# Kernel tuning notes

Measured on AMD Instinct MI355X. Metric: run time of the kernel, lower is better.

Reference implementation:

```python
import jax, jax.numpy as jnp
import numpy as np

B, T, C, H = 8, 2048, 1024, 128

def setup_inputs() -> dict:
    key = jax.random.key(0)
    kx, kq, kk, kv = jax.random.split(key, 4)
    x = jax.random.normal(kx, (B, T, C), dtype=jnp.float32)
    # torch nn.Linear(C, H, bias=False) computes x @ W.T with W of shape [H, C];
    # we store the transposed [C, H] matrices directly.
    Wq = jax.random.normal(kq, (C, H), dtype=jnp.float32) * (C ** -0.5)
    Wk = jax.random.normal(kk, (C, H), dtype=jnp.float32) * (C ** -0.5)
    Wv = jax.random.normal(kv, (C, H), dtype=jnp.float32) * (C ** -0.5)
    return {"x": x, "Wq": Wq, "Wk": Wk, "Wv": Wv}

def reference(x, Wq, Wk, Wv):
    # x: [B,T,C]; projections: [B,T,H]
    q = jnp.einsum('btc,ch->bth', x, Wq)
    k = jnp.einsum('btc,ch->bth', x, Wk)
    v = jnp.einsum('btc,ch->bth', x, Wv)
    scale = k.shape[-1] ** -0.5
    wei = jnp.einsum('bth,bsh->bts', q, k) * scale          # [B,T,T]
    # causal mask: position t attends to s <= t
    causal = jnp.tril(jnp.ones((x.shape[1], x.shape[1]), dtype=bool))
    wei = jnp.where(causal, wei, -jnp.inf)
    wei = jax.nn.softmax(wei, axis=-1)
    # dropout p=0.0 -> identity
    out = jnp.einsum('bts,bsh->bth', wei, v)                # [B,T,H]
    return out
```

## Files before the change

### kernel.cpp

```cpp
#include <hip/hip_runtime.h>
#include <hip/hip_bf16.h>

#define DB 8
#define DT 2048
#define DC 1024
#define DH 128

typedef __attribute__((ext_vector_type(8))) short short8;
typedef __attribute__((ext_vector_type(4))) float f32x4;
typedef __attribute__((ext_vector_type(4))) int i32x4;
typedef __attribute__((ext_vector_type(4))) unsigned short u16x4;

static __device__ __forceinline__ unsigned short bfbits(float x){
    union { float f; unsigned u; } a; a.f = x;
    unsigned u = a.u;
    unsigned r = u + 0x7fffu + ((u >> 16) & 1u);
    return (unsigned short)(r >> 16);
}
static __device__ __forceinline__ unsigned pbf2(float lo, float hi){
    return (unsigned)bfbits(lo) | ((unsigned)bfbits(hi) << 16);
}
static __device__ __forceinline__ float bf2f(unsigned short u){
    union { unsigned u; float f; } t; t.u = ((unsigned)u) << 16; return t.f;
}

static __device__ __forceinline__ short8 redist(unsigned pk0, unsigned pk1,
                                                unsigned pk2, unsigned pk3,
                                                int g, int c){
    const int src0 = c + (((2*g    ) & 3) << 4);
    const int src1 = c + (((2*g + 1) & 3) << 4);
    const int sel  = g >> 1;
    unsigned a0 = __shfl(pk0, src0), a2 = __shfl(pk2, src0);
    unsigned b0 = __shfl(pk1, src0), b2 = __shfl(pk3, src0);
    unsigned c0 = __shfl(pk0, src1), c2 = __shfl(pk2, src1);
    unsigned d0 = __shfl(pk1, src1), d2 = __shfl(pk3, src1);
    i32x4 pw = { (int)(sel ? a2 : a0), (int)(sel ? b2 : b0),
                 (int)(sel ? c2 : c0), (int)(sel ? d2 : d0) };
    return __builtin_bit_cast(short8, pw);
}

__global__ __launch_bounds__(256) void prep_wt_kernel(const float* __restrict__ Wq,
                                                      const float* __restrict__ Wk,
                                                      const float* __restrict__ Wv,
                                                      unsigned short* __restrict__ WTc){
    int gid = blockIdx.x * 256 + threadIdx.x;
    int e  = gid & 7;
    int F3 = gid >> 3;
    int n  = F3 % 384;
    int ct = F3 / 384;
    int k  = (ct >> 2) * 32 + (ct & 3) * 8 + e;
    int p  = n >> 7, h = n & 127;
    const float* W = (p == 0) ? Wq : (p == 1 ? Wk : Wv);
    float v = W[(size_t)k * DH + h];
    if (p == 0) v *= 0.08838834764831845f * 1.4426950408889634f;
    WTc[gid] = bfbits(v);
}

__global__ __launch_bounds__(512, 4) void qkv_kernel(const float* __restrict__ x,
                                                     const unsigned short* __restrict__ WTc,
                                                     unsigned short* __restrict__ Qb,
                                                     unsigned short* __restrict__ Kb,
                                                     unsigned short* __restrict__ VT){
    __shared__ unsigned short Bs[2][12288];
    __shared__ unsigned short As[2][2560];

    const int tid  = threadIdx.x;
    const int lane = tid & 63;
    const int w    = tid >> 6;
    const int g = lane >> 4, c = lane & 15;
    const int m0 = blockIdx.x * 64;
    const int n0 = w * 48;

    const unsigned short* bsrc = WTc + (size_t)tid * 8;
    const bool doA = tid < 256;
    const int arow = tid >> 2, ac8 = tid & 3;
    const float* asrc = x + (size_t)(m0 + arow) * DC + ac8 * 8;

    f32x4 acc[4][3] = {};
    i32x4 breg[3];
    float4 av0, av1;

#pragma unroll
    for (int j = 0; j < 3; ++j)
        breg[j] = *(const i32x4*)(bsrc + j * 4096);
    if (doA){ av0 = *(const float4*)asrc; av1 = *(const float4*)(asrc + 4); }
#pragma unroll
    for (int j = 0; j < 3; ++j)
        *(i32x4*)(&Bs[0][j * 4096 + tid * 8]) = breg[j];
    if (doA){
        i32x4 h8 = { (int)pbf2(av0.x, av0.y), (int)pbf2(av0.z, av0.w),
                     (int)pbf2(av1.x, av1.y), (int)pbf2(av1.z, av1.w) };
        *(i32x4*)(&As[0][arow * 40 + ac8 * 8]) = h8;
    }

    for (int t = 0; t < DC / 32; ++t){
        const int cur = t & 1;
        __syncthreads();
        if (t < DC / 32 - 1){
#pragma unroll
            for (int j = 0; j < 3; ++j)
                breg[j] = *(const i32x4*)(bsrc + (t + 1) * 12288 + j * 4096);
            if (doA){
                av0 = *(const float4*)(asrc + (t + 1) * 32);
                av1 = *(const float4*)(asrc + (t + 1) * 32 + 4);
            }
        }
        short8 af[4], bfr[3];
#pragma unroll
        for (int mf = 0; mf < 4; ++mf)
            af[mf] = *(const short8*)(&As[cur][(mf*16 + c) * 40 + g * 8]);
#pragma unroll
        for (int nf = 0; nf < 3; ++nf)
            bfr[nf] = *(const short8*)(&Bs[cur][g * 3072 + (n0 + nf*16 + c) * 8]);
#pragma unroll
        for (int mf = 0; mf < 4; ++mf)
#pragma unroll
            for (int nf = 0; nf < 3; ++nf)
                acc[mf][nf] = __builtin_amdgcn_mfma_f32_16x16x32_bf16(af[mf], bfr[nf], acc[mf][nf], 0, 0, 0);
        if (t < DC / 32 - 1){
#pragma unroll
            for (int j = 0; j < 3; ++j)
                *(i32x4*)(&Bs[cur ^ 1][j * 4096 + tid * 8]) = breg[j];
            if (doA){
                i32x4 h8 = { (int)pbf2(av0.x, av0.y), (int)pbf2(av0.z, av0.w),
                             (int)pbf2(av1.x, av1.y), (int)pbf2(av1.z, av1.w) };
                *(i32x4*)(&As[cur ^ 1][arow * 40 + ac8 * 8]) = h8;
            }
        }
    }

    const int bb = m0 >> 11;
    const int tb = m0 & 2047;
#pragma unroll
    for (int mf = 0; mf < 4; ++mf)
#pragma unroll
        for (int nf = 0; nf < 3; ++nf){
            const int n  = n0 + nf*16;
            const int p  = n >> 7;
            const int np = (n & 127) + c;
            const int row = m0 + mf*16 + 4*g;
            if (p < 2){
                unsigned short* O = (p == 0) ? Qb : Kb;
#pragma unroll
                for (int r = 0; r < 4; ++r)
                    O[(size_t)(row + r) * DH + np] = bfbits(acc[mf][nf][r]);
            } else {
                const int t0 = tb + mf*16 + 4*g;
                u16x4 v = { bfbits(acc[mf][nf][0]), bfbits(acc[mf][nf][1]),
                            bfbits(acc[mf][nf][2]), bfbits(acc[mf][nf][3]) };
                *(u16x4*)(VT + ((size_t)bb * DH + np) * DT + t0) = v;
            }
        }
}

__global__ __launch_bounds__(256, 2) void attn_kernel(const unsigned short* __restrict__ Qb,
                                                      const unsigned short* __restrict__ Kb,
                                                      const unsigned short* __restrict__ VT,
                                                      unsigned short* __restrict__ OP,
                                                      float* __restrict__ ML){
    __shared__ unsigned char lds[32768];

    const int tid  = threadIdx.x;
    const int lane = tid & 63;
    const int w    = tid >> 6;
    const int g = lane >> 4, c = lane & 15;
    const int bi = blockIdx.x;
    const int b  = bi & 7;
    const int idx = bi >> 3;
    const int qt   = (idx < 32) ? (31 - idx) : (idx - 32);
    const int half = idx >> 5;
    const int q0 = qt * 64;
    const int qw = q0 + 16 * w;
    const int q  = qw + c;
    const int nt = qt + 1;
    const int h1 = (nt + 1) >> 1;
    const int kt0 = half ? h1 : 0;
    const int kt1 = half ? nt : h1;

    const unsigned short* Kbase = Kb + (size_t)b * DT * DH;
    const unsigned short* Vbase = VT + (size_t)b * DH * DT;

    short8 qf[4];
#pragma unroll
    for (int hc = 0; hc < 4; ++hc)
        qf[hc] = *(const short8*)(Qb + ((size_t)b*DT + qw + c) * DH + hc*32 + g*8);

    f32x4 acc[8] = {};
    float m = -1e30f, l = 0.f;

    i32x4 kreg[4], vreg[4];
    if (kt0 < kt1){
        const int kv0 = kt0 * 64;
#pragma unroll
        for (int p = 0; p < 4; ++p){
            const int s = p*256 + tid;
            kreg[p] = *(const i32x4*)(Kbase + (size_t)(kv0 + (s >> 4)) * DH + (s & 15) * 8);
            vreg[p] = *(const i32x4*)(Vbase + (size_t)(s >> 3) * DT + kv0 + (s & 7) * 8);
        }
#pragma unroll
        for (int p = 0; p < 4; ++p){
            const int s = p*256 + tid;
            const int r = s >> 4, cb = (s & 15) * 16;
            *(i32x4*)(lds + r*256 + (cb ^ ((r & 7) << 4))) = kreg[p];
            const int h = s >> 3, tb = (s & 7) * 16;
            *(i32x4*)(lds + 16384 + h*128 + (tb ^ ((h & 7) << 4))) = vreg[p];
        }

        for (int kt = kt0; kt < kt1; ++kt){
            const int kv0c = kt * 64;
            __syncthreads();

            if (kt + 1 < kt1){
                const int nv0 = kv0c + 64;
#pragma unroll
                for (int p = 0; p < 4; ++p){
                    const int s = p*256 + tid;
                    kreg[p] = *(const i32x4*)(Kbase + (size_t)(nv0 + (s >> 4)) * DH + (s & 15) * 8);
                    vreg[p] = *(const i32x4*)(Vbase + (size_t)(s >> 3) * DT + nv0 + (s & 7) * 8);
                }
            }

            f32x4 s4[4] = {};
            short8 kf[4][4];
#pragma unroll
            for (int j = 0; j < 4; ++j){
                const int r = 16*j + c;
#pragma unroll
                for (int hc = 0; hc < 4; ++hc)
                    kf[j][hc] = *(const short8*)(lds + r*256 + ((hc*64 + g*16) ^ ((r & 7) << 4)));
            }
            __builtin_amdgcn_s_setprio(1);
#pragma unroll
            for (int hc = 0; hc < 4; ++hc)
#pragma unroll
                for (int j = 0; j < 4; ++j)
                    s4[j] = __builtin_amdgcn_mfma_f32_16x16x32_bf16(kf[j][hc], qf[hc], s4[j], 0,0,0);
            __builtin_amdgcn_s_setprio(0);

            if (kt == nt - 1){
#pragma unroll
                for (int j = 0; j < 4; ++j){
                    const int o = kv0c + 16*j + 4*g;
#pragma unroll
                    for (int r = 0; r < 4; ++r)
                        if (o + r > q) s4[j][r] = -1e30f;
                }
            }

            float tm = -1e30f;
#pragma unroll
            for (int j = 0; j < 4; ++j)
#pragma unroll
                for (int r = 0; r < 4; ++r) tm = fmaxf(tm, s4[j][r]);
            tm = fmaxf(tm, __shfl_xor(tm, 16));
            tm = fmaxf(tm, __shfl_xor(tm, 32));
            if (!__all(tm <= m + 8.f)){
                const float mn = fmaxf(m, tm);
                const float rs = exp2f(m - mn);
                l *= rs;
#pragma unroll
                for (int mt = 0; mt < 8; ++mt) acc[mt] *= rs;
                m = mn;
            }
            float p[4][4]; float ps = 0.f;
#pragma unroll
            for (int j = 0; j < 4; ++j)
#pragma unroll
                for (int r = 0; r < 4; ++r){
                    p[j][r] = exp2f(s4[j][r] - m);
                    ps += p[j][r];
                }
            ps += __shfl_xor(ps, 16);
            ps += __shfl_xor(ps, 32);
            l += ps;

            short8 pf0 = redist(pbf2(p[0][0], p[0][1]), pbf2(p[0][2], p[0][3]),
                                pbf2(p[1][0], p[1][1]), pbf2(p[1][2], p[1][3]), g, c);
            short8 pf1 = redist(pbf2(p[2][0], p[2][1]), pbf2(p[2][2], p[2][3]),
                                pbf2(p[3][0], p[3][1]), pbf2(p[3][2], p[3][3]), g, c);

#pragma unroll
            for (int kk = 0; kk < 2; ++kk){
                short8 vf[8];
#pragma unroll
                for (int mt = 0; mt < 8; ++mt){
                    const int h = mt*16 + c;
                    vf[mt] = *(const short8*)(lds + 16384 + h*128 + ((kk*64 + g*16) ^ ((h & 7) << 4)));
                }
                const short8 pf = kk ? pf1 : pf0;
                __builtin_amdgcn_s_setprio(1);
#pragma unroll
                for (int mt = 0; mt < 8; ++mt)
                    acc[mt] = __builtin_amdgcn_mfma_f32_16x16x32_bf16(vf[mt], pf, acc[mt], 0,0,0);
                __builtin_amdgcn_s_setprio(0);
            }

            __syncthreads();
            if (kt + 1 < kt1){
#pragma unroll
                for (int p2 = 0; p2 < 4; ++p2){
                    const int s = p2*256 + tid;
                    const int r = s >> 4, cb = (s & 15) * 16;
                    *(i32x4*)(lds + r*256 + (cb ^ ((r & 7) << 4))) = kreg[p2];
                    const int h = s >> 3, tb = (s & 7) * 16;
                    *(i32x4*)(lds + 16384 + h*128 + (tb ^ ((h & 7) << 4))) = vreg[p2];
                }
            }
        }
    }

    const size_t blk = ((size_t)(b * 32 + qt) * 2 + half);
    unsigned short* op = OP + blk * 8192;
    const int row = 16*w + c;
#pragma unroll
    for (int mt = 0; mt < 8; ++mt){
        u16x4 h = { bfbits(acc[mt][0]), bfbits(acc[mt][1]),
                    bfbits(acc[mt][2]), bfbits(acc[mt][3]) };
        *(u16x4*)(op + row*128 + mt*16 + 4*g) = h;
    }
    if (g == 0){
        ML[(blk*64 + row)*2    ] = m;
        ML[(blk*64 + row)*2 + 1] = l;
    }
}

__global__ __launch_bounds__(256) void merge_kernel(const unsigned short* __restrict__ OP,
                                                    const float* __restrict__ ML,
                                                    float* __restrict__ out){
    const int tid = threadIdx.x;
    const int r  = tid >> 2;
    const int cq = (tid & 3) * 32;
    const int bi = blockIdx.x;
    const int b  = bi & 7;
    const int qt = bi >> 3;
    const size_t blk = (size_t)(b * 32 + qt) * 2;

    float ms[2], ls[2];
#pragma unroll
    for (int s = 0; s < 2; ++s){
        ms[s] = ML[((blk + s)*64 + r)*2    ];
        ls[s] = ML[((blk + s)*64 + r)*2 + 1];
    }
    const float M = fmaxf(ms[0], ms[1]);
    float sc[2]; float L = 0.f;
#pragma unroll
    for (int s = 0; s < 2; ++s){ sc[s] = exp2f(ms[s] - M); L += ls[s] * sc[s]; }
    const float inv = 1.0f / L;

    float* orow = out + ((size_t)(b * DT + qt*64 + r)) * DH + cq;
#pragma unroll
    for (int j = 0; j < 4; ++j){
        float o[8] = {};
#pragma unroll
        for (int s = 0; s < 2; ++s){
            short8 v = *(const short8*)(OP + (blk + s)*8192 + r*128 + cq + j*8);
#pragma unroll
            for (int e = 0; e < 8; ++e)
                o[e] += bf2f((unsigned short)v[e]) * sc[s];
        }
        f32x4 o0 = { o[0]*inv, o[1]*inv, o[2]*inv, o[3]*inv };
        f32x4 o1 = { o[4]*inv, o[5]*inv, o[6]*inv, o[7]*inv };
        *(f32x4*)(orow + j*8    ) = o0;
        *(f32x4*)(orow + j*8 + 4) = o1;
    }
}

extern "C" void kernel_launch(void* const* d_in, const int* in_sizes, int n_in,
                              void* d_out, int out_size, void* d_ws, size_t ws_size,
                              hipStream_t stream){
    const float* x  = (const float*)d_in[0];
    const float* Wq = (const float*)d_in[1];
    const float* Wk = (const float*)d_in[2];
    const float* Wv = (const float*)d_in[3];
    float* out = (float*)d_out;

    unsigned short* WTc = (unsigned short*)d_ws;
    unsigned short* Qb = WTc + 3 * DH * DC;
    unsigned short* Kb = Qb + (size_t)DB * DT * DH;
    unsigned short* VT = Kb + (size_t)DB * DT * DH;
    unsigned short* OP = VT + (size_t)DB * DT * DH;
    float*          ML = (float*)(OP + (size_t)512 * 8192);

    hipLaunchKernelGGL(prep_wt_kernel, dim3(1536), dim3(256), 0, stream, Wq, Wk, Wv, WTc);
    hipLaunchKernelGGL(qkv_kernel, dim3(256), dim3(512), 0, stream, x, WTc, Qb, Kb, VT);
    hipLaunchKernelGGL(attn_kernel, dim3(512), dim3(256), 0, stream, Qb, Kb, VT, OP, ML);
    hipLaunchKernelGGL(merge_kernel, dim3(256), dim3(256), 0, stream, OP, ML, out);
}
```

Measured before the change: 81.11 us.

## Use direct global-to-LDS loads with double buffering in projection and attention

New measurement: 78.27 us. 1.04x faster.

```diff
diff --git a/kernel.cpp b/kernel.cpp
--- a/kernel.cpp
+++ b/kernel.cpp
@@ -22,6 +22,12 @@
 }
 static __device__ __forceinline__ float bf2f(unsigned short u){
     union { unsigned u; float f; } t; t.u = ((unsigned)u) << 16; return t.f;
+}
+
+static __device__ __forceinline__ void gload16(const void* g, void* l){
+    __builtin_amdgcn_global_load_lds(
+        (const __attribute__((address_space(1))) unsigned int*)g,
+        (__attribute__((address_space(3))) unsigned int*)l, 16, 0, 0);
 }
 
 static __device__ __forceinline__ short8 redist(unsigned pk0, unsigned pk1,
@@ -77,17 +83,13 @@
     const float* asrc = x + (size_t)(m0 + arow) * DC + ac8 * 8;
 
     f32x4 acc[4][3] = {};
-    i32x4 breg[3];
     float4 av0, av1;
 
 #pragma unroll
     for (int j = 0; j < 3; ++j)
-        breg[j] = *(const i32x4*)(bsrc + j * 4096);
-    if (doA){ av0 = *(const float4*)asrc; av1 = *(const float4*)(asrc + 4); }
-#pragma unroll
-    for (int j = 0; j < 3; ++j)
-        *(i32x4*)(&Bs[0][j * 4096 + tid * 8]) = breg[j];
+        gload16(bsrc + j * 4096, &Bs[0][j * 4096 + tid * 8]);
     if (doA){
+        av0 = *(const float4*)asrc; av1 = *(const float4*)(asrc + 4);
         i32x4 h8 = { (int)pbf2(av0.x, av0.y), (int)pbf2(av0.z, av0.w),
                      (int)pbf2(av1.x, av1.y), (int)pbf2(av1.z, av1.w) };
         *(i32x4*)(&As[0][arow * 40 + ac8 * 8]) = h8;
@@ -99,7 +101,8 @@
         if (t < DC / 32 - 1){
 #pragma unroll
             for (int j = 0; j < 3; ++j)
-                breg[j] = *(const i32x4*)(bsrc + (t + 1) * 12288 + j * 4096);
+                gload16(bsrc + (t + 1) * 12288 + j * 4096,
+                        &Bs[cur ^ 1][j * 4096 + tid * 8]);
             if (doA){
                 av0 = *(const float4*)(asrc + (t + 1) * 32);
                 av1 = *(const float4*)(asrc + (t + 1) * 32 + 4);
@@ -117,15 +120,10 @@
 #pragma unroll
             for (int nf = 0; nf < 3; ++nf)
                 acc[mf][nf] = __builtin_amdgcn_mfma_f32_16x16x32_bf16(af[mf], bfr[nf], acc[mf][nf], 0, 0, 0);
-        if (t < DC / 32 - 1){
-#pragma unroll
-            for (int j = 0; j < 3; ++j)
-                *(i32x4*)(&Bs[cur ^ 1][j * 4096 + tid * 8]) = breg[j];
-            if (doA){
-                i32x4 h8 = { (int)pbf2(av0.x, av0.y), (int)pbf2(av0.z, av0.w),
-                             (int)pbf2(av1.x, av1.y), (int)pbf2(av1.z, av1.w) };
-                *(i32x4*)(&As[cur ^ 1][arow * 40 + ac8 * 8]) = h8;
-            }
+        if (t < DC / 32 - 1 && doA){
+            i32x4 h8 = { (int)pbf2(av0.x, av0.y), (int)pbf2(av0.z, av0.w),
+                         (int)pbf2(av1.x, av1.y), (int)pbf2(av1.z, av1.w) };
+            *(i32x4*)(&As[cur ^ 1][arow * 40 + ac8 * 8]) = h8;
         }
     }
 
@@ -158,7 +156,7 @@
                                                       const unsigned short* __restrict__ VT,
                                                       unsigned short* __restrict__ OP,
                                                       float* __restrict__ ML){
-    __shared__ unsigned char lds[32768];
+    __shared__ unsigned char lds[2][32768];
 
     const int tid  = threadIdx.x;
     const int lane = tid & 63;
@@ -180,6 +178,8 @@
     const unsigned short* Kbase = Kb + (size_t)b * DT * DH;
     const unsigned short* Vbase = VT + (size_t)b * DH * DT;
 
+    const int sK_r[4]  = { (0*256 + tid) >> 4, (1*256 + tid) >> 4,
+                           (2*256 + tid) >> 4, (3*256 + tid) >> 4 };
     short8 qf[4];
 #pragma unroll
     for (int hc = 0; hc < 4; ++hc)
@@ -188,25 +188,23 @@
     f32x4 acc[8] = {};
     float m = -1e30f, l = 0.f;
 
-    i32x4 kreg[4], vreg[4];
     if (kt0 < kt1){
-        const int kv0 = kt0 * 64;
-#pragma unroll
-        for (int p = 0; p < 4; ++p){
-            const int s = p*256 + tid;
-            kreg[p] = *(const i32x4*)(Kbase + (size_t)(kv0 + (s >> 4)) * DH + (s & 15) * 8);
-            vreg[p] = *(const i32x4*)(Vbase + (size_t)(s >> 3) * DT + kv0 + (s & 7) * 8);
-        }
-#pragma unroll
-        for (int p = 0; p < 4; ++p){
-            const int s = p*256 + tid;
-            const int r = s >> 4, cb = (s & 15) * 16;
-            *(i32x4*)(lds + r*256 + (cb ^ ((r & 7) << 4))) = kreg[p];
-            const int h = s >> 3, tb = (s & 7) * 16;
-            *(i32x4*)(lds + 16384 + h*128 + (tb ^ ((h & 7) << 4))) = vreg[p];
+        {
+            const int kv0 = kt0 * 64;
+#pragma unroll
+            for (int p = 0; p < 4; ++p){
+                const int s = p*256 + tid;
+                const int r = s >> 4, cbl = (s & 15) * 16;
+                const int h = s >> 3, tbl = (s & 7) * 16;
+                gload16(Kbase + (size_t)(kv0 + r) * DH + ((cbl ^ ((r & 7) << 4)) >> 1),
+                        lds[0] + s*16);
+                gload16(Vbase + (size_t)h * DT + kv0 + ((tbl ^ ((h & 7) << 4)) >> 1),
+                        lds[0] + 16384 + s*16);
+            }
         }
 
         for (int kt = kt0; kt < kt1; ++kt){
+            const int cur = (kt - kt0) & 1;
             const int kv0c = kt * 64;
             __syncthreads();
 
@@ -215,10 +213,17 @@
 #pragma unroll
                 for (int p = 0; p < 4; ++p){
                     const int s = p*256 + tid;
-                    kreg[p] = *(const i32x4*)(Kbase + (size_t)(nv0 + (s >> 4)) * DH + (s & 15) * 8);
-                    vreg[p] = *(const i32x4*)(Vbase + (size_t)(s >> 3) * DT + nv0 + (s & 7) * 8);
+                    const int r = s >> 4, cbl = (s & 15) * 16;
+                    const int h = s >> 3, tbl = (s & 7) * 16;
+                    gload16(Kbase + (size_t)(nv0 + r) * DH + ((cbl ^ ((r & 7) << 4)) >> 1),
+                            lds[cur ^ 1] + s*16);
+                    gload16(Vbase + (size_t)h * DT + nv0 + ((tbl ^ ((h & 7) << 4)) >> 1),
+                            lds[cur ^ 1] + 16384 + s*16);
                 }
             }
+
+            const unsigned char* kb = lds[cur];
+            const unsigned char* vb = lds[cur] + 16384;
 
             f32x4 s4[4] = {};
             short8 kf[4][4];
@@ -227,7 +232,7 @@
                 const int r = 16*j + c;
 #pragma unroll
                 for (int hc = 0; hc < 4; ++hc)
-                    kf[j][hc] = *(const short8*)(lds + r*256 + ((hc*64 + g*16) ^ ((r & 7) << 4)));
+                    kf[j][hc] = *(const short8*)(kb + r*256 + ((hc*64 + g*16) ^ ((r & 7) << 4)));
             }
             __builtin_amdgcn_s_setprio(1);
 #pragma unroll
@@ -285,7 +290,7 @@
 #pragma unroll
                 for (int mt = 0; mt < 8; ++mt){
                     const int h = mt*16 + c;
-                    vf[mt] = *(const short8*)(lds + 16384 + h*128 + ((kk*64 + g*16) ^ ((h & 7) << 4)));
+                    vf[mt] = *(const short8*)(vb + h*128 + ((kk*64 + g*16) ^ ((h & 7) << 4)));
                 }
                 const short8 pf = kk ? pf1 : pf0;
                 __builtin_amdgcn_s_setprio(1);
@@ -293,18 +298,6 @@
                 for (int mt = 0; mt < 8; ++mt)
                     acc[mt] = __builtin_amdgcn_mfma_f32_16x16x32_bf16(vf[mt], pf, acc[mt], 0,0,0);
                 __builtin_amdgcn_s_setprio(0);
-            }
-
-            __syncthreads();
-            if (kt + 1 < kt1){
-#pragma unroll
-                for (int p2 = 0; p2 < 4; ++p2){
-                    const int s = p2*256 + tid;
-                    const int r = s >> 4, cb = (s & 15) * 16;
-                    *(i32x4*)(lds + r*256 + (cb ^ ((r & 7) << 4))) = kreg[p2];
-                    const int h = s >> 3, tb = (s & 7) * 16;
-                    *(i32x4*)(lds + 16384 + h*128 + (tb ^ ((h & 7) << 4))) = vreg[p2];
-                }
             }
         }
     }
```
